# Optimization experiments

Hardware: AMD Instinct MI355X
Metric: run time of the kernel (lower is better)

The kernel has to match this reference:

```python
import jax, jax.numpy as jnp
import numpy as np

DIM, KEY_DIM, HEADS, RATIO, RES = 384, 32, 8, 4, 7
N = RES * RES
D = RATIO * KEY_DIM          # 128 per-head value dim
DH = D * HEADS               # 1024
NHKD = KEY_DIM * HEADS       # 256
SCALE = KEY_DIM ** -0.5


def _make_bias_idxs(res):
    points = [(i, j) for i in range(res) for j in range(res)]
    offsets = {}
    idxs = []
    for p1 in points:
        for p2 in points:
            off = (abs(p1[0] - p2[0]), abs(p1[1] - p2[1]))
            if off not in offsets:
                offsets[off] = len(offsets)
            idxs.append(offsets[off])
    n = len(points)
    return np.asarray(idxs, dtype=np.int32).reshape(n, n), len(offsets)


def setup_inputs() -> dict:
    key = jax.random.key(0)
    ks = jax.random.split(key, 10)
    B = 2048
    idxs_np, n_off = _make_bias_idxs(RES)
    s = 0.02
    return {
        "x": jax.random.normal(ks[0], (B, N, DIM), jnp.float32),
        "q_w": jax.random.normal(ks[1], (NHKD, DIM), jnp.float32) * s,
        "q_b": jnp.zeros((NHKD,), jnp.float32),
        "k_w": jax.random.normal(ks[2], (NHKD, DIM), jnp.float32) * s,
        "k_b": jnp.zeros((NHKD,), jnp.float32),
        "v_w": jax.random.normal(ks[3], (DH, DIM), jnp.float32) * s,
        "v_b": jnp.zeros((DH,), jnp.float32),
        "proj_w": jax.random.normal(ks[4], (DIM, DH), jnp.float32) * s,
        "proj_b": jnp.zeros((DIM,), jnp.float32),
        "attention_biases": jax.random.normal(ks[5], (HEADS, n_off), jnp.float32) * s,
        "bias_idxs": jnp.asarray(idxs_np),  # [N, N] int32
    }


def reference(x, q_w, q_b, k_w, k_b, v_w, v_b, proj_w, proj_b,
              attention_biases, bias_idxs):
    B, n, _ = x.shape
    q = (x @ q_w.T + q_b).reshape(B, n, HEADS, KEY_DIM)
    k = (x @ k_w.T + k_b).reshape(B, n, HEADS, KEY_DIM)
    v = (x @ v_w.T + v_b).reshape(B, n, HEADS, D)
    # learned relative-position bias gathered per (query, key) pair: [H, N, N]
    ab = attention_biases[:, bias_idxs]
    attn = jnp.einsum("bnhd,bmhd->bhnm", q, k) * SCALE + ab
    attn = jax.nn.softmax(attn, axis=-1)
    out = jnp.einsum("bhnm,bmhd->bnhd", attn, v).reshape(B, n, DH)
    return out @ proj_w.T + proj_b
```

## Files before the change

### kernel.cpp

```cpp
#include <hip/hip_runtime.h>
#include <hip/hip_bf16.h>

#define NTOK   49
#define DIM    384
#define KEY_DIM 32
#define HEADS  8
#define D_HEAD 128
#define SCALE  0.17677669529663687f

typedef short short8 __attribute__((ext_vector_type(8)));
typedef short short4_t __attribute__((ext_vector_type(4)));
typedef float f32x4 __attribute__((ext_vector_type(4)));

__device__ __forceinline__ unsigned short f2bf(float x) {
    union { float f; unsigned u; } v; v.f = x;
    unsigned r = v.u + 0x7fffu + ((v.u >> 16) & 1u);
    return (unsigned short)(r >> 16);
}

__device__ __forceinline__ f32x4 MFMA(short8 a, short8 b, f32x4 c) {
    return __builtin_amdgcn_mfma_f32_16x16x32_bf16(a, b, c, 0, 0, 0);
}

__global__ void prologue(const float* __restrict__ qw, const float* __restrict__ qb,
                         const float* __restrict__ kw,
                         const float* __restrict__ vw, const float* __restrict__ pw,
                         const float* __restrict__ biases, const int* __restrict__ idxs,
                         int n_off,
                         unsigned short* __restrict__ qk_p,
                         unsigned short* __restrict__ vw_p,
                         unsigned short* __restrict__ pw_p,
                         float* __restrict__ qb_s,
                         float* __restrict__ ab_t) {
    int t = blockIdx.x * 256 + threadIdx.x;
    if (t < 24576) {
        int lane = t & 63, kt = (t >> 6) % 12, ntile = t / 768;
        int c = ntile * 16 + (lane & 15), kk = kt * 32 + (lane >> 4) * 8;
        const float* src = (c < 256) ? (qw + c * 384 + kk) : (kw + (c - 256) * 384 + kk);
        float sc = (c < 256) ? SCALE : 1.0f;
        short8 o;
#pragma unroll
        for (int j = 0; j < 8; ++j) o[j] = (short)f2bf(src[j] * sc);
        *(short8*)(qk_p + (size_t)t * 8) = o;
    } else if (t < 73728) {
        int u = t - 24576;
        int lane = u & 63, kt = (u >> 6) % 12, ntile = u / 768;
        int c = ntile * 16 + (lane & 15), kk = kt * 32 + (lane >> 4) * 8;
        const float* src = vw + c * 384 + kk;
        short8 o;
#pragma unroll
        for (int j = 0; j < 8; ++j) o[j] = (short)f2bf(src[j]);
        *(short8*)(vw_p + (size_t)u * 8) = o;
    } else if (t < 122880) {
        int u = t - 73728;
        int lane = u & 63, kt = (u >> 6) % 32, ntile = u / 2048;
        int c = ntile * 16 + (lane & 15), kk = kt * 32 + (lane >> 4) * 8;
        const float* src = pw + c * 1024 + kk;
        short8 o;
#pragma unroll
        for (int j = 0; j < 8; ++j) o[j] = (short)f2bf(src[j]);
        *(short8*)(pw_p + (size_t)u * 8) = o;
    } else if (t < 123136) {
        int u = t - 122880;
        qb_s[u] = qb[u] * SCALE;
    } else if (t < 123136 + 32768) {
        int u = t - 123136;
        int h = u >> 12, n = (u >> 6) & 63, m = u & 63;
        float v = 0.f;
        if (m < 49 && n < 49) v = biases[h * n_off + idxs[n * 49 + m]];
        ab_t[u] = v;
    }
}

__global__ __launch_bounds__(512, 4) void attn_qkv(
        const float* __restrict__ x,
        const unsigned short* __restrict__ qkw,
        const unsigned short* __restrict__ vw,
        const float* __restrict__ qb_s, const float* __restrict__ kb,
        const float* __restrict__ vb,
        const float* __restrict__ ab_t,
        unsigned short* __restrict__ O_p) {

    __shared__ __align__(16) unsigned short smem[37072];
    unsigned short* xs  = smem;
    unsigned short* ps  = smem + 19208;
    unsigned short* vsT = smem + 22736;
    unsigned short* qs  = smem + 31952;
    unsigned short* ks2 = smem + 34512;

    const int tid  = threadIdx.x;
    const int lane = tid & 63;
    const int wid  = tid >> 6;
    const int l15  = lane & 15;
    const int lg   = lane >> 4;
    const int b    = blockIdx.x;

    const float* xb = x + (size_t)b * (NTOK * DIM);
#pragma unroll 2
    for (int i = tid; i < 4704; i += 512) {
        f32x4 v = __builtin_nontemporal_load(((const f32x4*)xb) + i);
        int f = i * 4;
        int row = f / DIM;
        int col = f - row * DIM;
        short4_t pk;
        pk[0] = (short)f2bf(v[0]); pk[1] = (short)f2bf(v[1]);
        pk[2] = (short)f2bf(v[2]); pk[3] = (short)f2bf(v[3]);
        *(short4_t*)&xs[row * 392 + col] = pk;
    }
    __syncthreads();

    const f32x4 zf = (f32x4)0.f;

    for (int h = 0; h < HEADS; ++h) {
        {
            const int mh  = wid >> 2;
            const int nt0 = 3 * (wid & 3);
            const int rA0 = min(mh * 32 + l15, 48);
            const int rA1 = min(mh * 32 + 16 + l15, 48);
            f32x4 acc[3][2];
#pragma unroll
            for (int i = 0; i < 3; ++i) { acc[i][0] = zf; acc[i][1] = zf; }

            const short8* bptr[3];
#pragma unroll
            for (int i = 0; i < 3; ++i) {
                int nt = nt0 + i;
                const unsigned short* base; int ntile;
                if (nt < 2)      { base = qkw; ntile = 2 * h + nt; }
                else if (nt < 4) { base = qkw; ntile = 16 + 2 * h + (nt - 2); }
                else             { base = vw;  ntile = 8 * h + (nt - 4); }
                bptr[i] = (const short8*)(base + (size_t)ntile * 12 * 64 * 8);
            }
#pragma unroll
            for (int kt = 0; kt < 12; ++kt) {
                short8 a0 = *(const short8*)&xs[rA0 * 392 + kt * 32 + lg * 8];
                short8 a1 = *(const short8*)&xs[rA1 * 392 + kt * 32 + lg * 8];
#pragma unroll
                for (int i = 0; i < 3; ++i) {
                    short8 bf = bptr[i][kt * 64 + lane];
                    acc[i][0] = MFMA(a0, bf, acc[i][0]);
                    acc[i][1] = MFMA(a1, bf, acc[i][1]);
                }
            }
#pragma unroll
            for (int i = 0; i < 3; ++i) {
                int nt = nt0 + i;
                int c  = nt * 16 + l15;
                if (nt < 4) {
                    int cc = (nt < 2) ? c : c - 32;
                    float bias = (nt < 2) ? qb_s[h * 32 + cc] : kb[h * 32 + cc];
                    unsigned short* dst = (nt < 2) ? qs : ks2;
#pragma unroll
                    for (int j = 0; j < 2; ++j) {
                        int r0 = mh * 32 + j * 16 + lg * 4;
                        f32x4 v = acc[i][j];
#pragma unroll
                        for (int r = 0; r < 4; ++r)
                            dst[(r0 + r) * 40 + cc] = f2bf(v[r] + bias);
                    }
                } else {
                    int d = c - 64;
                    float bias = vb[h * 128 + d];
#pragma unroll
                    for (int j = 0; j < 2; ++j) {
                        int m0 = mh * 32 + j * 16 + lg * 4;
                        f32x4 v = acc[i][j];
                        short4_t pk;
#pragma unroll
                        for (int r = 0; r < 4; ++r) pk[r] = (short)f2bf(v[r] + bias);
                        *(short4_t*)&vsT[d * 72 + m0] = pk;
                    }
                }
            }
        }
        __syncthreads();

        if (wid < 4) {
            const int I = wid;
            const int rq = min(I * 16 + l15, 48);
            short8 bq = *(const short8*)&qs[rq * 40 + lg * 8];
            f32x4 s[4];
#pragma unroll
            for (int J = 0; J < 4; ++J) {
                short8 ak = *(const short8*)&ks2[(J * 16 + l15) * 40 + lg * 8];
                s[J] = MFMA(ak, bq, zf);
            }
            const f32x4* abn = (const f32x4*)(ab_t + ((h * 64 + I * 16 + l15) * 64));
            float sv[16];
            float mx = -1e30f;
#pragma unroll
            for (int J = 0; J < 4; ++J) {
                f32x4 a4 = abn[J * 4 + lg];
#pragma unroll
                for (int r = 0; r < 4; ++r) {
                    int m = J * 16 + lg * 4 + r;
                    float val = s[J][r] + a4[r];
                    if (m >= 49) val = -1e30f;
                    sv[J * 4 + r] = val;
                    mx = fmaxf(mx, val);
                }
            }
            mx = fmaxf(mx, __shfl_xor(mx, 16));
            mx = fmaxf(mx, __shfl_xor(mx, 32));
            float sum = 0.f;
#pragma unroll
            for (int t = 0; t < 16; ++t) { float e = __expf(sv[t] - mx); sv[t] = e; sum += e; }
            sum += __shfl_xor(sum, 16);
            sum += __shfl_xor(sum, 32);
            float inv = 1.0f / sum;
            int n = I * 16 + l15;
            if (n < 49) {
#pragma unroll
                for (int J = 0; J < 4; ++J)
#pragma unroll
                    for (int r = 0; r < 4; ++r) {
                        int m = J * 16 + lg * 4 + r;
                        ps[n * 72 + m] = f2bf(sv[J * 4 + r] * inv);
                    }
            }
        }
        __syncthreads();

        {
            const int np = wid >> 2;
            const int dp = wid & 3;
            const int rp0 = min(np * 32 + l15, 48);
            const int rp1 = min(np * 32 + 16 + l15, 48);
            f32x4 a00 = zf, a01 = zf, a10 = zf, a11 = zf;
#pragma unroll
            for (int kk = 0; kk < 2; ++kk) {
                short8 a0 = *(const short8*)&ps[rp0 * 72 + kk * 32 + lg * 8];
                short8 a1 = *(const short8*)&ps[rp1 * 72 + kk * 32 + lg * 8];
                short8 b0 = *(const short8*)&vsT[(dp * 32 + l15) * 72 + kk * 32 + lg * 8];
                short8 b1 = *(const short8*)&vsT[(dp * 32 + 16 + l15) * 72 + kk * 32 + lg * 8];
                a00 = MFMA(a0, b0, a00); a01 = MFMA(a0, b1, a01);
                a10 = MFMA(a1, b0, a10); a11 = MFMA(a1, b1, a11);
            }
            f32x4 accs[2][2] = {{a00, a01}, {a10, a11}};
            unsigned short* ob = O_p + (((size_t)b * 8 + h) * 32) * 256;
#pragma unroll
            for (int jn = 0; jn < 2; ++jn)
#pragma unroll
                for (int jd = 0; jd < 2; ++jd) {
                    int frag = (np * 2 + jn) * 8 + (dp * 2 + jd);
                    f32x4 v = accs[jn][jd];
                    short4_t pk;
#pragma unroll
                    for (int r = 0; r < 4; ++r) pk[r] = (short)f2bf(v[r]);
                    __builtin_nontemporal_store(pk, (short4_t*)(ob + frag * 256 + lane * 4));
                }
        }
        __syncthreads();
    }
}

__global__ __launch_bounds__(256) void out_proj(
        const unsigned short* __restrict__ O_p,
        const unsigned short* __restrict__ pw,
        const float* __restrict__ pb,
        float* __restrict__ out) {

    __shared__ __align__(16) unsigned short osB[64 * 136];

    const int tid  = threadIdx.x;
    const int lane = tid & 63;
    const int wid  = tid >> 6;
    const int l15  = lane & 15;
    const int lg   = lane >> 4;
    const int b    = blockIdx.x;

    f32x4 acc[6][4];
#pragma unroll
    for (int i = 0; i < 6; ++i)
#pragma unroll
        for (int j = 0; j < 4; ++j) acc[i][j] = (f32x4)0.f;

    for (int h = 0; h < HEADS; ++h) {
        const unsigned short* ob = O_p + (((size_t)b * 8 + h) * 32) * 256;
#pragma unroll
        for (int s = tid; s < 2048; s += 256) {
            int frag = s >> 6, ln = s & 63;
            short4_t v = __builtin_nontemporal_load((const short4_t*)(ob + frag * 256 + ln * 4));
            int mt = frag >> 3, dt = frag & 7;
            int r0 = mt * 16 + ((ln >> 4) << 2), c = dt * 16 + (ln & 15);
#pragma unroll
            for (int r = 0; r < 4; ++r) osB[(r0 + r) * 136 + c] = v[r];
        }
        __syncthreads();

#pragma unroll
        for (int kt = 0; kt < 4; ++kt) {
            short8 a[4];
#pragma unroll
            for (int mt = 0; mt < 4; ++mt)
                a[mt] = *(const short8*)&osB[(mt * 16 + l15) * 136 + kt * 32 + lg * 8];
#pragma unroll
            for (int i = 0; i < 6; ++i) {
                short8 bf = ((const short8*)pw)[((size_t)(wid * 6 + i) * 32 + (h * 4 + kt)) * 64 + lane];
#pragma unroll
                for (int mt = 0; mt < 4; ++mt)
                    acc[i][mt] = MFMA(a[mt], bf, acc[i][mt]);
            }
        }
        __syncthreads();
    }

    float* obase = out + (size_t)b * (NTOK * 384);
#pragma unroll
    for (int i = 0; i < 6; ++i) {
        int c = (wid * 6 + i) * 16 + l15;
        float bias = pb[c];
#pragma unroll
        for (int mt = 0; mt < 4; ++mt) {
            f32x4 v = acc[i][mt];
#pragma unroll
            for (int r = 0; r < 4; ++r) {
                int n = mt * 16 + lg * 4 + r;
                if (n < 49) __builtin_nontemporal_store(v[r] + bias, &obase[n * 384 + c]);
            }
        }
    }
}

__global__ __launch_bounds__(512) void fused_attn(
        const float* __restrict__ x,
        const unsigned short* __restrict__ qkw,
        const unsigned short* __restrict__ vw,
        const unsigned short* __restrict__ pw,
        const float* __restrict__ qb_s, const float* __restrict__ kb,
        const float* __restrict__ vb, const float* __restrict__ pb,
        const float* __restrict__ ab_t,
        float* __restrict__ out) {

    __shared__ __align__(16) unsigned short smem[40656];
    unsigned short* xs  = smem;
    unsigned short* ps  = smem + 19208;
    unsigned short* vsT = smem + 22736;
    unsigned short* qs  = smem + 31952;
    unsigned short* ks2 = smem + 31952 + 2560;
    unsigned short* osA = smem + 31952;

    const int tid  = threadIdx.x;
    const int lane = tid & 63;
    const int wid  = tid >> 6;
    const int l15  = lane & 15;
    const int lg   = lane >> 4;
    const int b    = blockIdx.x;

    const float* xb = x + (size_t)b * (NTOK * DIM);
#pragma unroll 2
    for (int i = tid; i < 4704; i += 512) {
        f32x4 v = __builtin_nontemporal_load(((const f32x4*)xb) + i);
        int f = i * 4;
        int row = f / DIM;
        int col = f - row * DIM;
        short4_t pk;
        pk[0] = (short)f2bf(v[0]); pk[1] = (short)f2bf(v[1]);
        pk[2] = (short)f2bf(v[2]); pk[3] = (short)f2bf(v[3]);
        *(short4_t*)&xs[row * 392 + col] = pk;
    }
    __syncthreads();

    f32x4 pacc[3][4];
#pragma unroll
    for (int i = 0; i < 3; ++i)
#pragma unroll
        for (int j = 0; j < 4; ++j) pacc[i][j] = (f32x4)0.f;

    const f32x4 zf = (f32x4)0.f;

    for (int h = 0; h < HEADS; ++h) {
        {
            const int mh  = wid >> 2;
            const int nt0 = 3 * (wid & 3);
            const int rA0 = min(mh * 32 + l15, 48);
            const int rA1 = min(mh * 32 + 16 + l15, 48);
            f32x4 acc[3][2];
#pragma unroll
            for (int i = 0; i < 3; ++i) { acc[i][0] = zf; acc[i][1] = zf; }

            const short8* bptr[3];
#pragma unroll
            for (int i = 0; i < 3; ++i) {
                int nt = nt0 + i;
                const unsigned short* base; int ntile;
                if (nt < 2)      { base = qkw; ntile = 2 * h + nt; }
                else if (nt < 4) { base = qkw; ntile = 16 + 2 * h + (nt - 2); }
                else             { base = vw;  ntile = 8 * h + (nt - 4); }
                bptr[i] = (const short8*)(base + (size_t)ntile * 12 * 64 * 8);
            }
#pragma unroll
            for (int kt = 0; kt < 12; ++kt) {
                short8 a0 = *(const short8*)&xs[rA0 * 392 + kt * 32 + lg * 8];
                short8 a1 = *(const short8*)&xs[rA1 * 392 + kt * 32 + lg * 8];
#pragma unroll
                for (int i = 0; i < 3; ++i) {
                    short8 bf = bptr[i][kt * 64 + lane];
                    acc[i][0] = MFMA(a0, bf, acc[i][0]);
                    acc[i][1] = MFMA(a1, bf, acc[i][1]);
                }
            }
#pragma unroll
            for (int i = 0; i < 3; ++i) {
                int nt = nt0 + i;
                int c  = nt * 16 + l15;
                if (nt < 4) {
                    int cc = (nt < 2) ? c : c - 32;
                    float bias = (nt < 2) ? qb_s[h * 32 + cc] : kb[h * 32 + cc];
                    unsigned short* dst = (nt < 2) ? qs : ks2;
#pragma unroll
                    for (int j = 0; j < 2; ++j) {
                        int r0 = mh * 32 + j * 16 + lg * 4;
                        f32x4 v = acc[i][j];
#pragma unroll
                        for (int r = 0; r < 4; ++r)
                            dst[(r0 + r) * 40 + cc] = f2bf(v[r] + bias);
                    }
                } else {
                    int d = c - 64;
                    float bias = vb[h * 128 + d];
#pragma unroll
                    for (int j = 0; j < 2; ++j) {
                        int m0 = mh * 32 + j * 16 + lg * 4;
                        f32x4 v = acc[i][j];
                        short4_t pk;
#pragma unroll
                        for (int r = 0; r < 4; ++r) pk[r] = (short)f2bf(v[r] + bias);
                        *(short4_t*)&vsT[d * 72 + m0] = pk;
                    }
                }
            }
        }
        __syncthreads();

        if (wid < 4) {
            const int I = wid;
            const int rq = min(I * 16 + l15, 48);
            short8 bq = *(const short8*)&qs[rq * 40 + lg * 8];
            f32x4 s[4];
#pragma unroll
            for (int J = 0; J < 4; ++J) {
                short8 ak = *(const short8*)&ks2[(J * 16 + l15) * 40 + lg * 8];
                s[J] = MFMA(ak, bq, zf);
            }
            const f32x4* abn = (const f32x4*)(ab_t + ((h * 64 + I * 16 + l15) * 64));
            float sv[16];
            float mx = -1e30f;
#pragma unroll
            for (int J = 0; J < 4; ++J) {
                f32x4 a4 = abn[J * 4 + lg];
#pragma unroll
                for (int r = 0; r < 4; ++r) {
                    int m = J * 16 + lg * 4 + r;
                    float val = s[J][r] + a4[r];
                    if (m >= 49) val = -1e30f;
                    sv[J * 4 + r] = val;
                    mx = fmaxf(mx, val);
                }
            }
            mx = fmaxf(mx, __shfl_xor(mx, 16));
            mx = fmaxf(mx, __shfl_xor(mx, 32));
            float sum = 0.f;
#pragma unroll
            for (int t = 0; t < 16; ++t) { float e = __expf(sv[t] - mx); sv[t] = e; sum += e; }
            sum += __shfl_xor(sum, 16);
            sum += __shfl_xor(sum, 32);
            float inv = 1.0f / sum;
            int n = I * 16 + l15;
            if (n < 49) {
#pragma unroll
                for (int J = 0; J < 4; ++J)
#pragma unroll
                    for (int r = 0; r < 4; ++r) {
                        int m = J * 16 + lg * 4 + r;
                        ps[n * 72 + m] = f2bf(sv[J * 4 + r] * inv);
                    }
            }
        }
        __syncthreads();

        {
            const int np = wid >> 2;
            const int dp = wid & 3;
            const int rp0 = min(np * 32 + l15, 48);
            const int rp1 = min(np * 32 + 16 + l15, 48);
            f32x4 a00 = zf, a01 = zf, a10 = zf, a11 = zf;
#pragma unroll
            for (int kk = 0; kk < 2; ++kk) {
                short8 a0 = *(const short8*)&ps[rp0 * 72 + kk * 32 + lg * 8];
                short8 a1 = *(const short8*)&ps[rp1 * 72 + kk * 32 + lg * 8];
                short8 b0 = *(const short8*)&vsT[(dp * 32 + l15) * 72 + kk * 32 + lg * 8];
                short8 b1 = *(const short8*)&vsT[(dp * 32 + 16 + l15) * 72 + kk * 32 + lg * 8];
                a00 = MFMA(a0, b0, a00); a01 = MFMA(a0, b1, a01);
                a10 = MFMA(a1, b0, a10); a11 = MFMA(a1, b1, a11);
            }
            f32x4 accs[2][2] = {{a00, a01}, {a10, a11}};
#pragma unroll
            for (int jn = 0; jn < 2; ++jn)
#pragma unroll
                for (int jd = 0; jd < 2; ++jd) {
                    int r0 = np * 32 + jn * 16 + lg * 4;
                    int d0 = dp * 32 + jd * 16 + l15;
                    f32x4 v = accs[jn][jd];
#pragma unroll
                    for (int r = 0; r < 4; ++r) osA[(r0 + r) * 136 + d0] = f2bf(v[r]);
                }
        }
        __syncthreads();

        {
            const int nt0 = 3 * wid;
#pragma unroll
            for (int kt = 0; kt < 4; ++kt) {
                short8 a[4];
#pragma unroll
                for (int mi = 0; mi < 4; ++mi)
                    a[mi] = *(const short8*)&osA[(mi * 16 + l15) * 136 + kt * 32 + lg * 8];
#pragma unroll
                for (int i = 0; i < 3; ++i) {
                    short8 bf = ((const short8*)pw)[((size_t)(nt0 + i) * 32 + (h * 4 + kt)) * 64 + lane];
#pragma unroll
                    for (int mi = 0; mi < 4; ++mi)
                        pacc[i][mi] = MFMA(a[mi], bf, pacc[i][mi]);
                }
            }
        }
        __syncthreads();
    }

    float* ob = out + (size_t)b * (NTOK * 384);
#pragma unroll
    for (int i = 0; i < 3; ++i) {
        int c = (3 * wid + i) * 16 + l15;
        float bias = pb[c];
#pragma unroll
        for (int mi = 0; mi < 4; ++mi) {
            f32x4 v = pacc[i][mi];
#pragma unroll
            for (int r = 0; r < 4; ++r) {
                int n = mi * 16 + lg * 4 + r;
                if (n < 49) __builtin_nontemporal_store(v[r] + bias, &ob[n * 384 + c]);
            }
        }
    }
}

extern "C" void kernel_launch(void* const* d_in, const int* in_sizes, int n_in,
                              void* d_out, int out_size, void* d_ws, size_t ws_size,
                              hipStream_t stream) {
    const float* x      = (const float*)d_in[0];
    const float* qw     = (const float*)d_in[1];
    const float* qb     = (const float*)d_in[2];
    const float* kw     = (const float*)d_in[3];
    const float* kb     = (const float*)d_in[4];
    const float* vw     = (const float*)d_in[5];
    const float* vb     = (const float*)d_in[6];
    const float* pw     = (const float*)d_in[7];
    const float* pb     = (const float*)d_in[8];
    const float* biases = (const float*)d_in[9];
    const int*   idxs   = (const int*)d_in[10];
    int n_off = in_sizes[9] / HEADS;

    char* ws = (char*)d_ws;
    unsigned short* qk_p = (unsigned short*)ws;
    unsigned short* vw_p = (unsigned short*)(ws + 393216);
    unsigned short* pw_p = (unsigned short*)(ws + 1179648);
    float*          qb_s = (float*)(ws + 1966080);
    float*          ab_t = (float*)(ws + 1967104);
    unsigned short* O_p  = (unsigned short*)(ws + 2098176);

    const size_t need = 2098176ull + (size_t)2048 * 8 * 32 * 256 * 2;

    prologue<<<609, 256, 0, stream>>>(qw, qb, kw, vw, pw, biases, idxs, n_off,
                                      qk_p, vw_p, pw_p, qb_s, ab_t);
    if (ws_size >= need) {
        attn_qkv<<<2048, 512, 0, stream>>>(x, qk_p, vw_p, qb_s, kb, vb, ab_t, O_p);
        out_proj<<<2048, 256, 0, stream>>>(O_p, pw_p, pb, (float*)d_out);
    } else {
        fused_attn<<<2048, 512, 0, stream>>>(x, qk_p, vw_p, pw_p, qb_s, kb, vb, pb,
                                             ab_t, (float*)d_out);
    }
}
```

Baseline: 478.3 us.

## Write attention output in MFMA operand layout and drop LDS staging in out_proj

attn_qkv now stages each head's output tile in shared memory and writes it to the intermediate buffer already packed as short8 MFMA operand fragments. out_proj can then read operands straight from global memory with a software-prefetched double buffer, with no LDS staging or per-head barriers. It also swaps operand roles so each thread writes f32x4 vectors to the output. The cost is a larger LDS footprint in attn_qkv plus an extra barrier and LDS round trip per head, which may cut occupancy there.

```diff
diff --git a/kernel.cpp b/kernel.cpp
--- a/kernel.cpp
+++ b/kernel.cpp
@@ -81,12 +81,13 @@
         const float* __restrict__ ab_t,
         unsigned short* __restrict__ O_p) {
 
-    __shared__ __align__(16) unsigned short smem[37072];
+    __shared__ __align__(16) unsigned short smem[40656];
     unsigned short* xs  = smem;
     unsigned short* ps  = smem + 19208;
     unsigned short* vsT = smem + 22736;
     unsigned short* qs  = smem + 31952;
     unsigned short* ks2 = smem + 34512;
+    unsigned short* osA = smem + 31952;
 
     const int tid  = threadIdx.x;
     const int lane = tid & 63;
@@ -237,30 +238,39 @@
                 a10 = MFMA(a1, b0, a10); a11 = MFMA(a1, b1, a11);
             }
             f32x4 accs[2][2] = {{a00, a01}, {a10, a11}};
-            unsigned short* ob = O_p + (((size_t)b * 8 + h) * 32) * 256;
 #pragma unroll
             for (int jn = 0; jn < 2; ++jn)
 #pragma unroll
                 for (int jd = 0; jd < 2; ++jd) {
-                    int frag = (np * 2 + jn) * 8 + (dp * 2 + jd);
+                    int r0 = np * 32 + jn * 16 + lg * 4;
+                    int d0 = dp * 32 + jd * 16 + l15;
                     f32x4 v = accs[jn][jd];
-                    short4_t pk;
-#pragma unroll
-                    for (int r = 0; r < 4; ++r) pk[r] = (short)f2bf(v[r]);
-                    __builtin_nontemporal_store(pk, (short4_t*)(ob + frag * 256 + lane * 4));
-                }
-        }
-        __syncthreads();
-    }
-}
-
-__global__ __launch_bounds__(256) void out_proj(
+#pragma unroll
+                    for (int r = 0; r < 4; ++r) osA[(r0 + r) * 136 + d0] = f2bf(v[r]);
+                }
+        }
+        __syncthreads();
+
+        {
+#pragma unroll
+            for (int q = 0; q < 2; ++q) {
+                int p   = wid * 2 + q;
+                int I   = p >> 2;
+                int ktl = p & 3;
+                short8 v = *(const short8*)&osA[(I * 16 + l15) * 136 + ktl * 32 + lg * 8];
+                __builtin_nontemporal_store(v,
+                    (short8*)(O_p + ((((size_t)b * 4 + I) * 32 + h * 4 + ktl) * 64 + lane) * 8));
+            }
+        }
+        __syncthreads();
+    }
+}
+
+__global__ void out_proj(
         const unsigned short* __restrict__ O_p,
         const unsigned short* __restrict__ pw,
         const float* __restrict__ pb,
         float* __restrict__ out) {
-
-    __shared__ __align__(16) unsigned short osB[64 * 136];
 
     const int tid  = threadIdx.x;
     const int lane = tid & 63;
@@ -269,54 +279,51 @@
     const int lg   = lane >> 4;
     const int b    = blockIdx.x;
 
+    const short8* ob  = (const short8*)O_p + (size_t)b * 4 * 32 * 64;
+    const short8* pwp = (const short8*)pw;
+
     f32x4 acc[6][4];
 #pragma unroll
     for (int i = 0; i < 6; ++i)
 #pragma unroll
-        for (int j = 0; j < 4; ++j) acc[i][j] = (f32x4)0.f;
-
-    for (int h = 0; h < HEADS; ++h) {
-        const unsigned short* ob = O_p + (((size_t)b * 8 + h) * 32) * 256;
-#pragma unroll
-        for (int s = tid; s < 2048; s += 256) {
-            int frag = s >> 6, ln = s & 63;
-            short4_t v = __builtin_nontemporal_load((const short4_t*)(ob + frag * 256 + ln * 4));
-            int mt = frag >> 3, dt = frag & 7;
-            int r0 = mt * 16 + ((ln >> 4) << 2), c = dt * 16 + (ln & 15);
-#pragma unroll
-            for (int r = 0; r < 4; ++r) osB[(r0 + r) * 136 + c] = v[r];
-        }
-        __syncthreads();
-
-#pragma unroll
-        for (int kt = 0; kt < 4; ++kt) {
-            short8 a[4];
-#pragma unroll
-            for (int mt = 0; mt < 4; ++mt)
-                a[mt] = *(const short8*)&osB[(mt * 16 + l15) * 136 + kt * 32 + lg * 8];
-#pragma unroll
-            for (int i = 0; i < 6; ++i) {
-                short8 bf = ((const short8*)pw)[((size_t)(wid * 6 + i) * 32 + (h * 4 + kt)) * 64 + lane];
-#pragma unroll
-                for (int mt = 0; mt < 4; ++mt)
-                    acc[i][mt] = MFMA(a[mt], bf, acc[i][mt]);
-            }
-        }
-        __syncthreads();
+        for (int I = 0; I < 4; ++I) acc[i][I] = (f32x4)0.f;
+
+    short8 bA[4], bB[4];
+#pragma unroll
+    for (int I = 0; I < 4; ++I) bA[I] = ob[(size_t)(I * 32 + 0) * 64 + lane];
+
+    for (int kt2 = 0; kt2 < 16; ++kt2) {
+        const int ktE = kt2 * 2, ktO = ktE + 1;
+#pragma unroll
+        for (int I = 0; I < 4; ++I) bB[I] = ob[(size_t)(I * 32 + ktO) * 64 + lane];
+#pragma unroll
+        for (int i = 0; i < 6; ++i) {
+            short8 a = pwp[((size_t)(wid * 6 + i) * 32 + ktE) * 64 + lane];
+#pragma unroll
+            for (int I = 0; I < 4; ++I) acc[i][I] = MFMA(a, bA[I], acc[i][I]);
+        }
+        const int ktN = (ktO + 1 < 32) ? ktO + 1 : 31;
+#pragma unroll
+        for (int I = 0; I < 4; ++I) bA[I] = ob[(size_t)(I * 32 + ktN) * 64 + lane];
+#pragma unroll
+        for (int i = 0; i < 6; ++i) {
+            short8 a = pwp[((size_t)(wid * 6 + i) * 32 + ktO) * 64 + lane];
+#pragma unroll
+            for (int I = 0; I < 4; ++I) acc[i][I] = MFMA(a, bB[I], acc[i][I]);
+        }
     }
 
     float* obase = out + (size_t)b * (NTOK * 384);
 #pragma unroll
     for (int i = 0; i < 6; ++i) {
-        int c = (wid * 6 + i) * 16 + l15;
-        float bias = pb[c];
-#pragma unroll
-        for (int mt = 0; mt < 4; ++mt) {
-            f32x4 v = acc[i][mt];
-#pragma unroll
-            for (int r = 0; r < 4; ++r) {
-                int n = mt * 16 + lg * 4 + r;
-                if (n < 49) __builtin_nontemporal_store(v[r] + bias, &obase[n * 384 + c]);
+        int c0 = (wid * 6 + i) * 16 + lg * 4;
+        f32x4 bias4 = *(const f32x4*)&pb[c0];
+#pragma unroll
+        for (int I = 0; I < 4; ++I) {
+            int n = I * 16 + l15;
+            if (n < 49) {
+                f32x4 v = acc[i][I] + bias4;
+                __builtin_nontemporal_store(v, (f32x4*)&obase[n * 384 + c0]);
             }
         }
     }
@@ -569,7 +576,7 @@
     float*          ab_t = (float*)(ws + 1967104);
     unsigned short* O_p  = (unsigned short*)(ws + 2098176);
 
-    const size_t need = 2098176ull + (size_t)2048 * 8 * 32 * 256 * 2;
+    const size_t need = 2098176ull + (size_t)2048 * 4 * 32 * 64 * 8 * 2;
 
     prologue<<<609, 256, 0, stream>>>(qw, qb, kw, vw, pw, biases, idxs, n_off,
                                       qk_p, vw_p, pw_p, qb_s, ab_t);
```

Result: slower. 797.5 us (+66.7%).

## Restructure out_proj to stage all heads in LDS with 512 threads

Applied to the files above, without the earlier changes.

The output projection kernel now loads all eight heads of the attention output into shared memory at once, using a single barrier instead of two per head. It runs 512 threads, with each wave owning 3 output column tiles instead of 6. The MFMA operands are swapped so accumulators hold token-major rows, which lets the kernel write 16-byte vectorised float4 outputs with a vector bias load. This trades a much larger LDS footprint (about 132KB per block), which limits blocks per CU, for fewer synchronisations and wider loads and stores.

```diff
diff --git a/kernel.cpp b/kernel.cpp
--- a/kernel.cpp
+++ b/kernel.cpp
@@ -254,13 +254,14 @@
     }
 }
 
-__global__ __launch_bounds__(256) void out_proj(
+#define OPJ_STRIDE 1032
+__global__ __launch_bounds__(512, 2) void out_proj(
         const unsigned short* __restrict__ O_p,
         const unsigned short* __restrict__ pw,
         const float* __restrict__ pb,
         float* __restrict__ out) {
 
-    __shared__ __align__(16) unsigned short osB[64 * 136];
+    __shared__ unsigned short osB[64 * OPJ_STRIDE];
 
     const int tid  = threadIdx.x;
     const int lane = tid & 63;
@@ -269,54 +270,59 @@
     const int lg   = lane >> 4;
     const int b    = blockIdx.x;
 
-    f32x4 acc[6][4];
-#pragma unroll
-    for (int i = 0; i < 6; ++i)
-#pragma unroll
-        for (int j = 0; j < 4; ++j) acc[i][j] = (f32x4)0.f;
-
-    for (int h = 0; h < HEADS; ++h) {
-        const unsigned short* ob = O_p + (((size_t)b * 8 + h) * 32) * 256;
-#pragma unroll
-        for (int s = tid; s < 2048; s += 256) {
-            int frag = s >> 6, ln = s & 63;
-            short4_t v = __builtin_nontemporal_load((const short4_t*)(ob + frag * 256 + ln * 4));
-            int mt = frag >> 3, dt = frag & 7;
-            int r0 = mt * 16 + ((ln >> 4) << 2), c = dt * 16 + (ln & 15);
-#pragma unroll
-            for (int r = 0; r < 4; ++r) osB[(r0 + r) * 136 + c] = v[r];
-        }
-        __syncthreads();
-
-#pragma unroll
-        for (int kt = 0; kt < 4; ++kt) {
-            short8 a[4];
-#pragma unroll
-            for (int mt = 0; mt < 4; ++mt)
-                a[mt] = *(const short8*)&osB[(mt * 16 + l15) * 136 + kt * 32 + lg * 8];
-#pragma unroll
-            for (int i = 0; i < 6; ++i) {
-                short8 bf = ((const short8*)pw)[((size_t)(wid * 6 + i) * 32 + (h * 4 + kt)) * 64 + lane];
-#pragma unroll
-                for (int mt = 0; mt < 4; ++mt)
-                    acc[i][mt] = MFMA(a[mt], bf, acc[i][mt]);
-            }
-        }
-        __syncthreads();
-    }
-
-    float* obase = out + (size_t)b * (NTOK * 384);
-#pragma unroll
-    for (int i = 0; i < 6; ++i) {
-        int c = (wid * 6 + i) * 16 + l15;
-        float bias = pb[c];
-#pragma unroll
-        for (int mt = 0; mt < 4; ++mt) {
-            f32x4 v = acc[i][mt];
-#pragma unroll
-            for (int r = 0; r < 4; ++r) {
-                int n = mt * 16 + lg * 4 + r;
-                if (n < 49) __builtin_nontemporal_store(v[r] + bias, &obase[n * 384 + c]);
+    const short8* obase = (const short8*)(O_p + (size_t)b * 65536);
+#pragma unroll
+    for (int it = 0; it < 16; ++it) {
+        int s = tid + it * 512;
+        short8 v = __builtin_nontemporal_load(obase + s);
+        int fl0 = s * 2;
+        int h    = fl0 >> 11;
+        int frag = (fl0 >> 6) & 31;
+        int ln0  = fl0 & 63;
+        int mt = frag >> 3, dt = frag & 7;
+#pragma unroll
+        for (int p = 0; p < 2; ++p) {
+            int ln = ln0 + p;
+            int n0 = mt * 16 + ((ln >> 4) << 2);
+            int d  = h * 128 + dt * 16 + (ln & 15);
+#pragma unroll
+            for (int r = 0; r < 4; ++r)
+                osB[(n0 + r) * OPJ_STRIDE + d] = (unsigned short)v[p * 4 + r];
+        }
+    }
+    __syncthreads();
+
+    const short8* pwp = (const short8*)pw;
+    f32x4 acc[3][4];
+#pragma unroll
+    for (int i = 0; i < 3; ++i)
+#pragma unroll
+        for (int I = 0; I < 4; ++I) acc[i][I] = (f32x4)0.f;
+
+    for (int kt = 0; kt < 32; ++kt) {
+        short8 bfr[4];
+#pragma unroll
+        for (int I = 0; I < 4; ++I)
+            bfr[I] = *(const short8*)&osB[(I * 16 + l15) * OPJ_STRIDE + kt * 32 + lg * 8];
+#pragma unroll
+        for (int i = 0; i < 3; ++i) {
+            short8 a = pwp[((size_t)(wid * 3 + i) * 32 + kt) * 64 + lane];
+#pragma unroll
+            for (int I = 0; I < 4; ++I) acc[i][I] = MFMA(a, bfr[I], acc[i][I]);
+        }
+    }
+
+    float* obaseo = out + (size_t)b * (NTOK * 384);
+#pragma unroll
+    for (int i = 0; i < 3; ++i) {
+        int c0 = (wid * 3 + i) * 16 + lg * 4;
+        f32x4 bias4 = *(const f32x4*)&pb[c0];
+#pragma unroll
+        for (int I = 0; I < 4; ++I) {
+            int n = I * 16 + l15;
+            if (n < 49) {
+                f32x4 v = acc[i][I] + bias4;
+                __builtin_nontemporal_store(v, (f32x4*)&obaseo[n * 384 + c0]);
             }
         }
     }
@@ -575,7 +581,7 @@
                                       qk_p, vw_p, pw_p, qb_s, ab_t);
     if (ws_size >= need) {
         attn_qkv<<<2048, 512, 0, stream>>>(x, qk_p, vw_p, qb_s, kb, vb, ab_t, O_p);
-        out_proj<<<2048, 256, 0, stream>>>(O_p, pw_p, pb, (float*)d_out);
+        out_proj<<<2048, 512, 0, stream>>>(O_p, pw_p, pb, (float*)d_out);
     } else {
         fused_attn<<<2048, 512, 0, stream>>>(x, qk_p, vw_p, pw_p, qb_s, kb, vb, pb,
                                              ab_t, (float*)d_out);
```

Result: faster. 423.9 us (-11.4%).
